# Performance work log

Measured on AMD Instinct MI355X. Metric: run time of the kernel, lower is better.

## Reference

```python
import jax, jax.numpy as jnp
import numpy as np

B, K1, D, H = 512, 128, 512, 8
HD = D // H
LN_EPS = 1e-5


def setup_inputs() -> dict:
    key = jax.random.key(0)
    ks = jax.random.split(key, 8)
    x = jax.random.normal(ks[0], (B, K1, D), dtype=jnp.float32)
    corr_scores = jax.random.normal(ks[1], (B, K1), dtype=jnp.float32)
    peer_mask = jax.random.randint(ks[2], (B, K1), 0, 2) > 0
    # guarantee at least one valid (unmasked) slot per row so softmax rows are finite
    peer_mask = peer_mask.at[:, 0].set(False)
    # nn.MultiheadAttention parameters (packed in_proj, out_proj)
    s = 1.0 / np.sqrt(D)
    in_proj_w = jax.random.uniform(ks[3], (3 * D, D), minval=-s, maxval=s, dtype=jnp.float32)
    in_proj_b = jnp.zeros((3 * D,), dtype=jnp.float32)
    out_proj_w = jax.random.uniform(ks[4], (D, D), minval=-s, maxval=s, dtype=jnp.float32)
    out_proj_b = jnp.zeros((D,), dtype=jnp.float32)
    ln_w = jnp.ones((D,), dtype=jnp.float32)
    ln_b = jnp.zeros((D,), dtype=jnp.float32)
    bias_scale = jnp.asarray(1.0, dtype=jnp.float32)
    return {
        'x': x, 'corr_scores': corr_scores, 'peer_mask': peer_mask,
        'in_proj_w': in_proj_w, 'in_proj_b': in_proj_b,
        'out_proj_w': out_proj_w, 'out_proj_b': out_proj_b,
        'ln_w': ln_w, 'ln_b': ln_b, 'bias_scale': bias_scale,
    }


def reference(x, corr_scores, peer_mask, in_proj_w, in_proj_b,
              out_proj_w, out_proj_b, ln_w, ln_b, bias_scale):
    b, L, d = x.shape
    qkv = x @ in_proj_w.T + in_proj_b  # (B, L, 3D)
    q, k, v = jnp.split(qkv, 3, axis=-1)
    # (B, H, L, HD)
    q = q.reshape(b, L, H, HD).transpose(0, 2, 1, 3) * (HD ** -0.5)
    k = k.reshape(b, L, H, HD).transpose(0, 2, 1, 3)
    v = v.reshape(b, L, H, HD).transpose(0, 2, 1, 3)
    scores = jnp.einsum('bhld,bhsd->bhls', q, k)  # (B, H, L, L)
    # additive correlation bias, same for every head and every query row
    bias = bias_scale * corr_scores[:, None, None, :]  # (B, 1, 1, L)
    bias = jnp.where(peer_mask[:, None, None, :], -jnp.inf, bias)
    attn = jax.nn.softmax(scores + bias, axis=-1)
    o = jnp.einsum('bhls,bhsd->bhld', attn, v)  # (B, H, L, HD)
    o = o.transpose(0, 2, 1, 3).reshape(b, L, d)
    attn_out = o @ out_proj_w.T + out_proj_b
    # residual + LayerNorm
    h = x + attn_out
    mu = jnp.mean(h, axis=-1, keepdims=True)
    var = jnp.mean(jnp.square(h - mu), axis=-1, keepdims=True)
    out = (h - mu) * jax.lax.rsqrt(var + LN_EPS) * ln_w + ln_b
    return out
```

## Files before the change

kernel.cpp:

```cpp
#include <hip/hip_runtime.h>
#include <hip/hip_bf16.h>
#include <math.h>


typedef __attribute__((ext_vector_type(4))) float f32x4;
typedef __attribute__((ext_vector_type(8))) short bf16x8;

__device__ __forceinline__ unsigned short f2bf(float f) {
  union { float f; unsigned u; } x; x.f = f;
  return (unsigned short)((x.u + 0x7FFFu + ((x.u >> 16) & 1u)) >> 16);
}

__device__ __forceinline__ void gload16(const void* g, void* l) {
  __builtin_amdgcn_global_load_lds((const __attribute__((address_space(1))) void*)g,
                                   (__attribute__((address_space(3))) void*)l, 16, 0, 0);
}

__global__ void cvt_f32_bf16(const float* __restrict__ in,
                             unsigned short* __restrict__ out, int n8) {
  int i = blockIdx.x * blockDim.x + threadIdx.x;
  if (i >= n8) return;
  const float4* p = (const float4*)in + (size_t)i * 2;
  float4 a = p[0], b = p[1];
  union { bf16x8 v; short s[8]; } o;
  o.s[0] = (short)f2bf(a.x); o.s[1] = (short)f2bf(a.y);
  o.s[2] = (short)f2bf(a.z); o.s[3] = (short)f2bf(a.w);
  o.s[4] = (short)f2bf(b.x); o.s[5] = (short)f2bf(b.y);
  o.s[6] = (short)f2bf(b.z); o.s[7] = (short)f2bf(b.w);
  *(bf16x8*)(out + (size_t)i * 8) = o.v;
}

template <int MODE, int NBX>
__global__ __launch_bounds__(256, 3) void gemm_lds(
    const unsigned short* __restrict__ A, const unsigned short* __restrict__ Bt,
    unsigned short* __restrict__ Cb, float* __restrict__ Cf,
    const float* __restrict__ bias, const float* __restrict__ resid, int ldC) {
  __shared__ __align__(16) unsigned short As[128 * 64];
  __shared__ __align__(16) unsigned short Bs[128 * 64];
  const int t = threadIdx.x;
  const int w = t >> 6, lane = t & 63;
  const int wr = w >> 1, wc = w & 1;
  const int g = lane >> 4, l16 = lane & 15;
  const int bid = blockIdx.x;
  const int cpx = (int)(gridDim.x >> 3);
  const int nid = (bid & 7) * cpx + (bid >> 3);
  const long rowBase = (long)(nid / NBX) * 128;
  const long colBase = (long)(nid % NBX) * 128;

  f32x4 acc[4][4] = {};

  for (int k0 = 0; k0 < 512; k0 += 64) {
#pragma unroll
    for (int i = 0; i < 4; ++i) {
      int flat = i * 256 + t;
      int row = flat >> 3;
      int c8 = ((flat & 7) ^ (row & 7)) << 3;
      gload16(A + (rowBase + row) * 512 + k0 + c8, (char*)As + flat * 16);
      gload16(Bt + (colBase + row) * 512 + k0 + c8, (char*)Bs + flat * 16);
    }
    __syncthreads();
#pragma unroll
    for (int kk = 0; kk < 2; ++kk) {
      bf16x8 af[4], bfr[4];
#pragma unroll
      for (int fm = 0; fm < 4; ++fm) {
        int r = wr * 64 + fm * 16 + l16;
        af[fm] = *(const bf16x8*)((char*)As + r * 128 + ((kk * 64 + g * 16) ^ ((r & 7) << 4)));
      }
#pragma unroll
      for (int fn = 0; fn < 4; ++fn) {
        int r = wc * 64 + fn * 16 + l16;
        bfr[fn] = *(const bf16x8*)((char*)Bs + r * 128 + ((kk * 64 + g * 16) ^ ((r & 7) << 4)));
      }
#pragma unroll
      for (int fm = 0; fm < 4; ++fm)
#pragma unroll
        for (int fn = 0; fn < 4; ++fn)
          acc[fm][fn] = __builtin_amdgcn_mfma_f32_16x16x32_bf16(af[fm], bfr[fn], acc[fm][fn], 0, 0, 0);
    }
    __syncthreads();
  }

#pragma unroll
  for (int fm = 0; fm < 4; ++fm) {
#pragma unroll
    for (int fn = 0; fn < 4; ++fn) {
      long col = colBase + wc * 64 + fn * 16 + l16;
      float bcol = bias[col];
#pragma unroll
      for (int r = 0; r < 4; ++r) {
        long row = rowBase + wr * 64 + fm * 16 + g * 4 + r;
        float v = acc[fm][fn][r] + bcol;
        if constexpr (MODE == 0) {
          if (col < 512) v *= 0.125f;
          Cb[row * ldC + col] = f2bf(v);
        } else {
          Cf[row * ldC + col] = v + resid[row * ldC + col];
        }
      }
    }
  }
}

__global__ __launch_bounds__(256, 2) void attn_kernel(
    const unsigned short* __restrict__ qkv, const float* __restrict__ corr,
    const int* __restrict__ mask, const float* __restrict__ bias_scale,
    unsigned short* __restrict__ o) {
  __shared__ __align__(16) unsigned short Pl[4][32 * 136];
  __shared__ __align__(16) unsigned short vt[64 * 136];
  __shared__ float biasl[128];
  const int t = threadIdx.x;
  const int w = t >> 6, lane = t & 63;
  const int g = lane >> 4, l16 = lane & 15;
  const int b = blockIdx.x >> 3, h = blockIdx.x & 7;
  const long qkvBase = (long)b * 128 * 1536;

#pragma unroll
  for (int i = 0; i < 4; ++i) {
    int q = t + i * 256;
    int row = q >> 3, c8 = q & 7;
    union { bf16x8 v; unsigned short s[8]; } u;
    u.v = *(const bf16x8*)(qkv + qkvBase + (long)row * 1536 + 1024 + h * 64 + c8 * 8);
#pragma unroll
    for (int j = 0; j < 8; ++j) vt[(c8 * 8 + j) * 136 + row] = u.s[j];
  }
  if (t < 128) {
    float bs = bias_scale[0];
    biasl[t] = mask[b * 128 + t] ? -INFINITY : bs * corr[b * 128 + t];
  }

  bf16x8 aq[2][2], bk[8][2];
#pragma unroll
  for (int fm = 0; fm < 2; ++fm)
#pragma unroll
    for (int kk = 0; kk < 2; ++kk)
      aq[fm][kk] = *(const bf16x8*)(qkv + qkvBase + (long)(w * 32 + fm * 16 + l16) * 1536 + h * 64 + kk * 32 + g * 8);
#pragma unroll
  for (int fn = 0; fn < 8; ++fn)
#pragma unroll
    for (int kk = 0; kk < 2; ++kk)
      bk[fn][kk] = *(const bf16x8*)(qkv + qkvBase + (long)(fn * 16 + l16) * 1536 + 512 + h * 64 + kk * 32 + g * 8);

  __syncthreads();

  f32x4 accS[2][8] = {};
#pragma unroll
  for (int kk = 0; kk < 2; ++kk)
#pragma unroll
    for (int fm = 0; fm < 2; ++fm)
#pragma unroll
      for (int fn = 0; fn < 8; ++fn)
        accS[fm][fn] = __builtin_amdgcn_mfma_f32_16x16x32_bf16(aq[fm][kk], bk[fn][kk], accS[fm][fn], 0, 0, 0);

  float bv[8];
#pragma unroll
  for (int fn = 0; fn < 8; ++fn) bv[fn] = biasl[fn * 16 + l16];

  float rinv[2][4];
#pragma unroll
  for (int fm = 0; fm < 2; ++fm) {
#pragma unroll
    for (int r = 0; r < 4; ++r) {
      float m = -INFINITY;
#pragma unroll
      for (int fn = 0; fn < 8; ++fn) m = fmaxf(m, accS[fm][fn][r] + bv[fn]);
#pragma unroll
      for (int off = 1; off < 16; off <<= 1) m = fmaxf(m, __shfl_xor(m, off));
      float s = 0.f;
#pragma unroll
      for (int fn = 0; fn < 8; ++fn) {
        float p = __expf(accS[fm][fn][r] + bv[fn] - m);
        accS[fm][fn][r] = p;
        s += p;
      }
#pragma unroll
      for (int off = 1; off < 16; off <<= 1) s += __shfl_xor(s, off);
      rinv[fm][r] = 1.0f / s;
#pragma unroll
      for (int fn = 0; fn < 8; ++fn)
        Pl[w][(fm * 16 + g * 4 + r) * 136 + fn * 16 + l16] = f2bf(accS[fm][fn][r]);
    }
  }

  f32x4 accO[2][4] = {};
#pragma unroll
  for (int kk = 0; kk < 4; ++kk) {
    bf16x8 ap[2], bw[4];
#pragma unroll
    for (int fm = 0; fm < 2; ++fm)
      ap[fm] = *(const bf16x8*)&Pl[w][(fm * 16 + l16) * 136 + kk * 32 + g * 8];
#pragma unroll
    for (int fn = 0; fn < 4; ++fn)
      bw[fn] = *(const bf16x8*)&vt[(fn * 16 + l16) * 136 + kk * 32 + g * 8];
#pragma unroll
    for (int fm = 0; fm < 2; ++fm)
#pragma unroll
      for (int fn = 0; fn < 4; ++fn)
        accO[fm][fn] = __builtin_amdgcn_mfma_f32_16x16x32_bf16(ap[fm], bw[fn], accO[fm][fn], 0, 0, 0);
  }

  const long oBase = (long)b * 128 * 512 + (long)h * 64;
#pragma unroll
  for (int fm = 0; fm < 2; ++fm)
#pragma unroll
    for (int fn = 0; fn < 4; ++fn)
#pragma unroll
      for (int r = 0; r < 4; ++r)
        o[oBase + (long)(w * 32 + fm * 16 + g * 4 + r) * 512 + fn * 16 + l16] =
            f2bf(accO[fm][fn][r] * rinv[fm][r]);
}

__global__ __launch_bounds__(256) void ln_kernel(float* __restrict__ h,
                                                 const float* __restrict__ lnw,
                                                 const float* __restrict__ lnb) {
  const int t = threadIdx.x;
  const int w = t >> 6, lane = t & 63;
  const long row = (long)blockIdx.x * 4 + w;
  float* rp = h + row * 512;
  float4 v0 = *(float4*)(rp + lane * 4);
  float4 v1 = *(float4*)(rp + 256 + lane * 4);
  float s = ((v0.x + v0.y) + (v0.z + v0.w)) + ((v1.x + v1.y) + (v1.z + v1.w));
#pragma unroll
  for (int off = 1; off < 64; off <<= 1) s += __shfl_xor(s, off);
  float mu = s * (1.0f / 512.0f);
  float vs = (v0.x - mu) * (v0.x - mu) + (v0.y - mu) * (v0.y - mu) +
             (v0.z - mu) * (v0.z - mu) + (v0.w - mu) * (v0.w - mu) +
             (v1.x - mu) * (v1.x - mu) + (v1.y - mu) * (v1.y - mu) +
             (v1.z - mu) * (v1.z - mu) + (v1.w - mu) * (v1.w - mu);
#pragma unroll
  for (int off = 1; off < 64; off <<= 1) vs += __shfl_xor(vs, off);
  float rstd = rsqrtf(vs * (1.0f / 512.0f) + 1e-5f);
  float4 w0 = *(const float4*)(lnw + lane * 4);
  float4 w1 = *(const float4*)(lnw + 256 + lane * 4);
  float4 b0 = *(const float4*)(lnb + lane * 4);
  float4 b1 = *(const float4*)(lnb + 256 + lane * 4);
  float4 o0, o1;
  o0.x = (v0.x - mu) * rstd * w0.x + b0.x;
  o0.y = (v0.y - mu) * rstd * w0.y + b0.y;
  o0.z = (v0.z - mu) * rstd * w0.z + b0.z;
  o0.w = (v0.w - mu) * rstd * w0.w + b0.w;
  o1.x = (v1.x - mu) * rstd * w1.x + b1.x;
  o1.y = (v1.y - mu) * rstd * w1.y + b1.y;
  o1.z = (v1.z - mu) * rstd * w1.z + b1.z;
  o1.w = (v1.w - mu) * rstd * w1.w + b1.w;
  *(float4*)(rp + lane * 4) = o0;
  *(float4*)(rp + 256 + lane * 4) = o1;
}

extern "C" void kernel_launch(void* const* d_in, const int* in_sizes, int n_in,
                              void* d_out, int out_size, void* d_ws, size_t ws_size,
                              hipStream_t stream) {
  const float* x = (const float*)d_in[0];
  const float* corr = (const float*)d_in[1];
  const int* mask = (const int*)d_in[2];
  const float* w_in = (const float*)d_in[3];
  const float* b_in = (const float*)d_in[4];
  const float* w_out = (const float*)d_in[5];
  const float* b_out = (const float*)d_in[6];
  const float* ln_w = (const float*)d_in[7];
  const float* ln_b = (const float*)d_in[8];
  const float* bscale = (const float*)d_in[9];

  unsigned short* wqkv_bf = (unsigned short*)d_ws;
  unsigned short* wout_bf = wqkv_bf + 786432;
  unsigned short* qkv = wout_bf + 262144;
  unsigned short* xb_ob = qkv + (size_t)65536 * 1536;

  cvt_f32_bf16<<<dim3(384), dim3(256), 0, stream>>>(w_in, wqkv_bf, 98304);
  cvt_f32_bf16<<<dim3(128), dim3(256), 0, stream>>>(w_out, wout_bf, 32768);
  cvt_f32_bf16<<<dim3(16384), dim3(256), 0, stream>>>(x, xb_ob, 4194304);

  gemm_lds<0, 12><<<dim3(6144), dim3(256), 0, stream>>>(
      xb_ob, wqkv_bf, qkv, (float*)nullptr, b_in, (const float*)nullptr, 1536);

  attn_kernel<<<dim3(4096), dim3(256), 0, stream>>>(qkv, corr, mask, bscale, xb_ob);

  gemm_lds<1, 4><<<dim3(2048), dim3(256), 0, stream>>>(
      xb_ob, wout_bf, (unsigned short*)nullptr, (float*)d_out, b_out, x, 512);

  ln_kernel<<<dim3(16384), dim3(256), 0, stream>>>((float*)d_out, ln_w, ln_b);
}
```

Baseline: 608.6 us.

## Fuse output projection with residual LayerNorm and stage K through LDS in attention

Replaces the separate out-projection GEMM and LayerNorm kernels with one kernel in which each block computes full 512-wide rows (128x512 tile) and applies bias, residual and LayerNorm in registers. This removes the fp32 round trip of the intermediate through global memory and one launch. Row statistics use a sum/sum-of-squares variance, which is less numerically robust. The attention kernel now loads K into swizzled LDS with global_load_lds instead of direct per-lane global loads. The fused kernel launches only 512 blocks of 512 threads with one block per CU, so occupancy and latency hiding drop, and its single-buffered K loop has no load/compute overlap.

```diff
diff --git a/kernel.cpp b/kernel.cpp
--- a/kernel.cpp
+++ b/kernel.cpp
@@ -102,10 +102,128 @@
   }
 }
 
+__global__ __launch_bounds__(512, 1) void oproj_ln(
+    const unsigned short* __restrict__ Ab, const unsigned short* __restrict__ Wt,
+    const float* __restrict__ x, const float* __restrict__ bout,
+    const float* __restrict__ lnw, const float* __restrict__ lnb,
+    float* __restrict__ out) {
+  __shared__ __align__(16) unsigned short As[128 * 64];
+  __shared__ __align__(16) unsigned short Bs[512 * 64];
+  __shared__ float ps[128][4], pq[128][4], mus[128], rss[128];
+  const int t = threadIdx.x;
+  const int w = t >> 6, lane = t & 63;
+  const int wr = w >> 2, wc = w & 3;
+  const int g = lane >> 4, l16 = lane & 15;
+  const long rowBase = (long)blockIdx.x * 128;
+
+  f32x4 acc[4][8] = {};
+
+  for (int k0 = 0; k0 < 512; k0 += 64) {
+#pragma unroll
+    for (int i = 0; i < 2; ++i) {
+      int flat = i * 512 + t;
+      int row = flat >> 3;
+      int c8 = ((flat & 7) ^ (row & 7)) << 3;
+      gload16(Ab + (rowBase + row) * 512 + k0 + c8, (char*)As + flat * 16);
+    }
+#pragma unroll
+    for (int i = 0; i < 8; ++i) {
+      int flat = i * 512 + t;
+      int row = flat >> 3;
+      int c8 = ((flat & 7) ^ (row & 7)) << 3;
+      gload16(Wt + row * 512 + k0 + c8, (char*)Bs + flat * 16);
+    }
+    __syncthreads();
+#pragma unroll
+    for (int kk = 0; kk < 2; ++kk) {
+      bf16x8 af[4], bfr[8];
+#pragma unroll
+      for (int fm = 0; fm < 4; ++fm) {
+        int r = wr * 64 + fm * 16 + l16;
+        af[fm] = *(const bf16x8*)((char*)As + r * 128 + ((kk * 64 + g * 16) ^ ((r & 7) << 4)));
+      }
+#pragma unroll
+      for (int fn = 0; fn < 8; ++fn) {
+        int n = wc * 128 + fn * 16 + l16;
+        bfr[fn] = *(const bf16x8*)((char*)Bs + n * 128 + ((kk * 64 + g * 16) ^ ((n & 7) << 4)));
+      }
+#pragma unroll
+      for (int fm = 0; fm < 4; ++fm)
+#pragma unroll
+        for (int fn = 0; fn < 8; ++fn)
+          acc[fm][fn] = __builtin_amdgcn_mfma_f32_16x16x32_bf16(af[fm], bfr[fn], acc[fm][fn], 0, 0, 0);
+    }
+    __syncthreads();
+  }
+
+  float bo[8];
+#pragma unroll
+  for (int fn = 0; fn < 8; ++fn) bo[fn] = bout[wc * 128 + fn * 16 + l16];
+
+#pragma unroll
+  for (int fm = 0; fm < 4; ++fm) {
+#pragma unroll
+    for (int r = 0; r < 4; ++r) {
+      const int rloc = wr * 64 + fm * 16 + g * 4 + r;
+      const long row = rowBase + rloc;
+      float sh = 0.f, sq = 0.f;
+#pragma unroll
+      for (int fn = 0; fn < 8; ++fn) {
+        int col = wc * 128 + fn * 16 + l16;
+        float h = acc[fm][fn][r] + bo[fn] + x[row * 512 + col];
+        acc[fm][fn][r] = h;
+        sh += h;
+        sq += h * h;
+      }
+#pragma unroll
+      for (int off = 1; off < 16; off <<= 1) {
+        sh += __shfl_xor(sh, off);
+        sq += __shfl_xor(sq, off);
+      }
+      if (l16 == 0) {
+        ps[rloc][wc] = sh;
+        pq[rloc][wc] = sq;
+      }
+    }
+  }
+  __syncthreads();
+  if (t < 128) {
+    float s = ps[t][0] + ps[t][1] + ps[t][2] + ps[t][3];
+    float q = pq[t][0] + pq[t][1] + pq[t][2] + pq[t][3];
+    float mu = s * (1.0f / 512.0f);
+    float var = q * (1.0f / 512.0f) - mu * mu;
+    mus[t] = mu;
+    rss[t] = rsqrtf(var + 1e-5f);
+  }
+  __syncthreads();
+
+  float lw[8], lb[8];
+#pragma unroll
+  for (int fn = 0; fn < 8; ++fn) {
+    lw[fn] = lnw[wc * 128 + fn * 16 + l16];
+    lb[fn] = lnb[wc * 128 + fn * 16 + l16];
+  }
+#pragma unroll
+  for (int fm = 0; fm < 4; ++fm) {
+#pragma unroll
+    for (int r = 0; r < 4; ++r) {
+      const int rloc = wr * 64 + fm * 16 + g * 4 + r;
+      const long row = rowBase + rloc;
+      const float mu = mus[rloc], rs = rss[rloc];
+#pragma unroll
+      for (int fn = 0; fn < 8; ++fn) {
+        int col = wc * 128 + fn * 16 + l16;
+        out[row * 512 + col] = (acc[fm][fn][r] - mu) * rs * lw[fn] + lb[fn];
+      }
+    }
+  }
+}
+
 __global__ __launch_bounds__(256, 2) void attn_kernel(
     const unsigned short* __restrict__ qkv, const float* __restrict__ corr,
     const int* __restrict__ mask, const float* __restrict__ bias_scale,
     unsigned short* __restrict__ o) {
+  __shared__ __align__(16) unsigned short kt[128 * 64];
   __shared__ __align__(16) unsigned short Pl[4][32 * 136];
   __shared__ __align__(16) unsigned short vt[64 * 136];
   __shared__ float biasl[128];
@@ -117,6 +235,14 @@
 
 #pragma unroll
   for (int i = 0; i < 4; ++i) {
+    int flat = i * 256 + t;
+    int row = flat >> 3;
+    int c8 = ((flat & 7) ^ (row & 7)) << 3;
+    gload16(qkv + qkvBase + (long)row * 1536 + 512 + h * 64 + c8, (char*)kt + flat * 16);
+  }
+
+#pragma unroll
+  for (int i = 0; i < 4; ++i) {
     int q = t + i * 256;
     int row = q >> 3, c8 = q & 7;
     union { bf16x8 v; unsigned short s[8]; } u;
@@ -129,28 +255,27 @@
     biasl[t] = mask[b * 128 + t] ? -INFINITY : bs * corr[b * 128 + t];
   }
 
-  bf16x8 aq[2][2], bk[8][2];
+  bf16x8 aq[2][2];
 #pragma unroll
   for (int fm = 0; fm < 2; ++fm)
 #pragma unroll
     for (int kk = 0; kk < 2; ++kk)
       aq[fm][kk] = *(const bf16x8*)(qkv + qkvBase + (long)(w * 32 + fm * 16 + l16) * 1536 + h * 64 + kk * 32 + g * 8);
-#pragma unroll
-  for (int fn = 0; fn < 8; ++fn)
-#pragma unroll
-    for (int kk = 0; kk < 2; ++kk)
-      bk[fn][kk] = *(const bf16x8*)(qkv + qkvBase + (long)(fn * 16 + l16) * 1536 + 512 + h * 64 + kk * 32 + g * 8);
 
   __syncthreads();
 
   f32x4 accS[2][8] = {};
 #pragma unroll
-  for (int kk = 0; kk < 2; ++kk)
-#pragma unroll
-    for (int fm = 0; fm < 2; ++fm)
-#pragma unroll
-      for (int fn = 0; fn < 8; ++fn)
-        accS[fm][fn] = __builtin_amdgcn_mfma_f32_16x16x32_bf16(aq[fm][kk], bk[fn][kk], accS[fm][fn], 0, 0, 0);
+  for (int fn = 0; fn < 8; ++fn) {
+    int r = fn * 16 + l16;
+    bf16x8 bk0 = *(const bf16x8*)((char*)kt + r * 128 + ((g * 16) ^ ((r & 7) << 4)));
+    bf16x8 bk1 = *(const bf16x8*)((char*)kt + r * 128 + ((64 + g * 16) ^ ((r & 7) << 4)));
+#pragma unroll
+    for (int fm = 0; fm < 2; ++fm) {
+      accS[fm][fn] = __builtin_amdgcn_mfma_f32_16x16x32_bf16(aq[fm][0], bk0, accS[fm][fn], 0, 0, 0);
+      accS[fm][fn] = __builtin_amdgcn_mfma_f32_16x16x32_bf16(aq[fm][1], bk1, accS[fm][fn], 0, 0, 0);
+    }
+  }
 
   float bv[8];
 #pragma unroll
@@ -208,43 +333,6 @@
       for (int r = 0; r < 4; ++r)
         o[oBase + (long)(w * 32 + fm * 16 + g * 4 + r) * 512 + fn * 16 + l16] =
             f2bf(accO[fm][fn][r] * rinv[fm][r]);
-}
-
-__global__ __launch_bounds__(256) void ln_kernel(float* __restrict__ h,
-                                                 const float* __restrict__ lnw,
-                                                 const float* __restrict__ lnb) {
-  const int t = threadIdx.x;
-  const int w = t >> 6, lane = t & 63;
-  const long row = (long)blockIdx.x * 4 + w;
-  float* rp = h + row * 512;
-  float4 v0 = *(float4*)(rp + lane * 4);
-  float4 v1 = *(float4*)(rp + 256 + lane * 4);
-  float s = ((v0.x + v0.y) + (v0.z + v0.w)) + ((v1.x + v1.y) + (v1.z + v1.w));
-#pragma unroll
-  for (int off = 1; off < 64; off <<= 1) s += __shfl_xor(s, off);
-  float mu = s * (1.0f / 512.0f);
-  float vs = (v0.x - mu) * (v0.x - mu) + (v0.y - mu) * (v0.y - mu) +
-             (v0.z - mu) * (v0.z - mu) + (v0.w - mu) * (v0.w - mu) +
-             (v1.x - mu) * (v1.x - mu) + (v1.y - mu) * (v1.y - mu) +
-             (v1.z - mu) * (v1.z - mu) + (v1.w - mu) * (v1.w - mu);
-#pragma unroll
-  for (int off = 1; off < 64; off <<= 1) vs += __shfl_xor(vs, off);
-  float rstd = rsqrtf(vs * (1.0f / 512.0f) + 1e-5f);
-  float4 w0 = *(const float4*)(lnw + lane * 4);
-  float4 w1 = *(const float4*)(lnw + 256 + lane * 4);
-  float4 b0 = *(const float4*)(lnb + lane * 4);
-  float4 b1 = *(const float4*)(lnb + 256 + lane * 4);
-  float4 o0, o1;
-  o0.x = (v0.x - mu) * rstd * w0.x + b0.x;
-  o0.y = (v0.y - mu) * rstd * w0.y + b0.y;
-  o0.z = (v0.z - mu) * rstd * w0.z + b0.z;
-  o0.w = (v0.w - mu) * rstd * w0.w + b0.w;
-  o1.x = (v1.x - mu) * rstd * w1.x + b1.x;
-  o1.y = (v1.y - mu) * rstd * w1.y + b1.y;
-  o1.z = (v1.z - mu) * rstd * w1.z + b1.z;
-  o1.w = (v1.w - mu) * rstd * w1.w + b1.w;
-  *(float4*)(rp + lane * 4) = o0;
-  *(float4*)(rp + 256 + lane * 4) = o1;
 }
 
 extern "C" void kernel_launch(void* const* d_in, const int* in_sizes, int n_in,
@@ -275,8 +363,6 @@
 
   attn_kernel<<<dim3(4096), dim3(256), 0, stream>>>(qkv, corr, mask, bscale, xb_ob);
 
-  gemm_lds<1, 4><<<dim3(2048), dim3(256), 0, stream>>>(
-      xb_ob, wout_bf, (unsigned short*)nullptr, (float*)d_out, b_out, x, 512);
-
-  ln_kernel<<<dim3(16384), dim3(256), 0, stream>>>((float*)d_out, ln_w, ln_b);
-}
+  oproj_ln<<<dim3(512), dim3(512), 0, stream>>>(
+      xb_ob, wout_bf, x, b_out, ln_w, ln_b, (float*)d_out);
+}
```

New measurement: 534.2 us. 1.14x faster.
